# Performance work log

Hardware: AMD Instinct MI355X
Metric: run time of the kernel (lower is better)

## Reference

```python
import jax, jax.numpy as jnp
import numpy as np

N = 50000   # number of nodes
E = 25000   # number of hyperedges
IN = 256
OUT = 256
L = 32      # incidence list width (padded with 0)
NEG = -9e15  # matches torch's -9000000000000000.0 (fits in fp32)


def setup_inputs() -> dict:
    key = jax.random.key(0)
    k1, k2, k3, k4, k5 = jax.random.split(key, 5)
    x = jax.random.normal(k1, (N, IN), dtype=jnp.float32)
    seq = jax.random.randint(k2, (E, L), 0, N)      # node ids per hyperedge
    useq = jax.random.randint(k3, (N, L), 0, E)     # edge ids per node
    stdv = 1.0 / np.sqrt(IN)
    W1 = jax.random.uniform(k4, (IN, OUT), minval=-stdv, maxval=stdv, dtype=jnp.float32)
    W2 = jax.random.uniform(k5, (OUT, OUT), minval=-stdv, maxval=stdv, dtype=jnp.float32)
    return {"x": x, "seq": seq, "useq": useq, "W1": W1, "W2": W2}


def _mask_softmax_weights(idx):
    # softmax over where(idx>0, 1, -9e15): uniform weights over non-padding slots
    logits = jnp.where(idx > 0, 1.0, NEG).astype(jnp.float32)
    return jax.nn.softmax(logits, axis=1)


def reference(x, seq, useq, W1, W2):
    x1 = x @ W1                                   # [N, OUT]
    w = _mask_softmax_weights(seq)                # [E, L]
    edge = jnp.einsum('elc,el->ec', x1[seq], w)   # gather + weighted reduce -> [E, OUT]
    # F.dropout is identity in eval mode
    edge = jax.nn.relu(edge)
    e1 = edge @ W2                                # [E, OUT]
    uw = _mask_softmax_weights(useq)              # [N, L]
    node = jnp.einsum('nlc,nl->nc', e1[useq], uw) # [N, OUT]
    return node
```

## Files before the change

### kernel.cpp

```cpp
#include <hip/hip_runtime.h>

constexpr int N_NODES = 50000;
constexpr int N_EDGES = 25000;
constexpr int C = 256;
constexpr int L = 32;

__device__ ushort W1T_g[C * C];
__device__ ushort W2T_g[C * C];

__device__ __forceinline__ float bf2f(unsigned int h) {
    union { unsigned int u; float f; } c; c.u = h << 16; return c.f;
}
__device__ __forceinline__ ushort f2bf(float f) {
    union { float f; unsigned int u; } c; c.f = f;
    unsigned int r = c.u + 0x7FFFu + ((c.u >> 16) & 1u);
    return (ushort)(r >> 16);
}

__global__ __launch_bounds__(256) void convert_x_kernel(
    const float* __restrict__ x, ushort* __restrict__ xb)
{
    const size_t i = ((size_t)blockIdx.x * 256 + threadIdx.x) * 4;
    const float4 v = *reinterpret_cast<const float4*>(x + i);
    ushort4 o;
    o.x = f2bf(v.x); o.y = f2bf(v.y); o.z = f2bf(v.z); o.w = f2bf(v.w);
    *reinterpret_cast<ushort4*>(xb + i) = o;
}

__global__ __launch_bounds__(256) void wconv_kernel(
    const float* __restrict__ W1, const float* __restrict__ W2)
{
    const float* W  = blockIdx.z ? W2 : W1;
    ushort* WT      = blockIdx.z ? W2T_g : W1T_g;
    __shared__ float t[64][65];
    const int rr = threadIdx.x >> 6;
    const int cc = threadIdx.x & 63;
    const int br = blockIdx.x * 64;
    const int bc = blockIdx.y * 64;
#pragma unroll
    for (int i = 0; i < 16; ++i) {
        const int row = i * 4 + rr;
        t[row][cc] = W[(size_t)(br + row) * C + bc + cc];
    }
    __syncthreads();
#pragma unroll
    for (int i = 0; i < 16; ++i) {
        const int n = i * 4 + rr;
        WT[(size_t)(bc + n) * C + br + cc] = f2bf(t[cc][n]);
    }
}

template <typename OutT>
__global__ __launch_bounds__(256) void gather_avg_kernel(
    const ushort* __restrict__ src, const int* __restrict__ idx,
    OutT* __restrict__ dst, int nrows)
{
    const int row = blockIdx.x * 8 + (threadIdx.x >> 5);
    const int ln  = threadIdx.x & 31;
    if (row >= nrows) return;

    const int myid = idx[(size_t)row * L + ln];
    const unsigned long long b = __ballot(myid > 0);
    const unsigned int halfmask = (unsigned int)(b >> (threadIdx.x & 32));
    const int cnt = __popc(halfmask);
    const bool all = (cnt == 0);
    const float w = all ? (1.0f / (float)L) : (1.0f / (float)cnt);

    float acc[8] = {0.f, 0.f, 0.f, 0.f, 0.f, 0.f, 0.f, 0.f};
#pragma unroll 4
    for (int l = 0; l < L; ++l) {
        const int id = __shfl(myid, l, 32);
        if (all || id > 0) {
            const uint4 v = *reinterpret_cast<const uint4*>(
                src + (size_t)id * C + ln * 8);
            acc[0] += bf2f(v.x & 0xFFFFu); acc[1] += bf2f(v.x >> 16);
            acc[2] += bf2f(v.y & 0xFFFFu); acc[3] += bf2f(v.y >> 16);
            acc[4] += bf2f(v.z & 0xFFFFu); acc[5] += bf2f(v.z >> 16);
            acc[6] += bf2f(v.w & 0xFFFFu); acc[7] += bf2f(v.w >> 16);
        }
    }

    if constexpr (sizeof(OutT) == 2) {
        ushort* d = (ushort*)dst + (size_t)row * C + ln * 8;
        ushort4 o0, o1;
        o0.x = f2bf(acc[0] * w); o0.y = f2bf(acc[1] * w);
        o0.z = f2bf(acc[2] * w); o0.w = f2bf(acc[3] * w);
        o1.x = f2bf(acc[4] * w); o1.y = f2bf(acc[5] * w);
        o1.z = f2bf(acc[6] * w); o1.w = f2bf(acc[7] * w);
        *reinterpret_cast<ushort4*>(d)     = o0;
        *reinterpret_cast<ushort4*>(d + 4) = o1;
    } else {
        float* d = (float*)dst + (size_t)row * C + ln * 8;
        float4 o0 = {acc[0] * w, acc[1] * w, acc[2] * w, acc[3] * w};
        float4 o1 = {acc[4] * w, acc[5] * w, acc[6] * w, acc[7] * w};
        *reinterpret_cast<float4*>(d)     = o0;
        *reinterpret_cast<float4*>(d + 4) = o1;
    }
}

typedef __attribute__((ext_vector_type(8))) short bf16x8;
typedef __attribute__((ext_vector_type(4))) float f32x4;

template <bool RELU>
__global__ __launch_bounds__(256) void gemm_mfma_kernel(
    const ushort* __restrict__ A, int which_w,
    ushort* __restrict__ Cmat, int M)
{
    const ushort* __restrict__ BT = which_w ? W2T_g : W1T_g;
    const int wave = threadIdx.x >> 6;
    const int lane = threadIdx.x & 63;
    const int quad = lane >> 4;
    const int l16  = lane & 15;
    const int base = (blockIdx.x * 4 + wave) * 16;
    int mc = base + l16; if (mc > M - 1) mc = M - 1;

    f32x4 acc[16];
    const f32x4 zero = {0.f, 0.f, 0.f, 0.f};
#pragma unroll
    for (int t = 0; t < 16; ++t) acc[t] = zero;

    const ushort* arow = A  + (size_t)mc  * C + quad * 8;
    const ushort* brow = BT + (size_t)l16 * C + quad * 8;

#pragma unroll
    for (int k0 = 0; k0 < C; k0 += 32) {
        const bf16x8 a = *reinterpret_cast<const bf16x8*>(arow + k0);
#pragma unroll
        for (int t = 0; t < 16; ++t) {
            const bf16x8 b = *reinterpret_cast<const bf16x8*>(
                brow + (size_t)t * 16 * C + k0);
            acc[t] = __builtin_amdgcn_mfma_f32_16x16x32_bf16(a, b, acc[t], 0, 0, 0);
        }
    }

#pragma unroll
    for (int t = 0; t < 16; ++t) {
#pragma unroll
        for (int r = 0; r < 4; ++r) {
            const int gm = base + quad * 4 + r;
            if (gm < M) {
                float v = acc[t][r];
                if (RELU) v = fmaxf(v, 0.f);
                Cmat[(size_t)gm * C + t * 16 + l16] = f2bf(v);
            }
        }
    }
}

extern "C" void kernel_launch(void* const* d_in, const int* in_sizes, int n_in,
                              void* d_out, int out_size, void* d_ws, size_t ws_size,
                              hipStream_t stream) {
    const float* x    = (const float*)d_in[0];
    const int*   seq  = (const int*)d_in[1];
    const int*   useq = (const int*)d_in[2];
    const float* W1   = (const float*)d_in[3];
    const float* W2   = (const float*)d_in[4];
    float* out = (float*)d_out;

    ushort* xb   = (ushort*)d_ws;
    ushort* tmp1 = xb + (size_t)N_NODES * C;
    ushort* edge = tmp1 + (size_t)N_EDGES * C;

    convert_x_kernel<<<dim3((N_NODES * C) / (256 * 4)), dim3(256), 0, stream>>>(x, xb);
    wconv_kernel<<<dim3(4, 4, 2), dim3(256), 0, stream>>>(W1, W2);

    gather_avg_kernel<ushort><<<dim3(N_EDGES / 8), dim3(256), 0, stream>>>(
        xb, seq, tmp1, N_EDGES);

    const dim3 ggrid((N_EDGES + 63) / 64);
    gemm_mfma_kernel<true><<<ggrid, dim3(256), 0, stream>>>(tmp1, 0, edge, N_EDGES);
    gemm_mfma_kernel<false><<<ggrid, dim3(256), 0, stream>>>(edge, 1, tmp1, N_EDGES);

    gather_avg_kernel<float><<<dim3(N_NODES / 8), dim3(256), 0, stream>>>(
        tmp1, useq, out, N_NODES);
}
```

Measured before the change: 320.1 us.

## Split gather-average into column chunks with shared-memory index staging

```diff
diff --git a/kernel.cpp b/kernel.cpp
--- a/kernel.cpp
+++ b/kernel.cpp
@@ -50,47 +50,74 @@
     }
 }
 
-template <typename OutT>
-__global__ __launch_bounds__(256) void gather_avg_kernel(
+template <int CH, int NCHUNK, typename OutT>
+__global__ __launch_bounds__(256) void gather_chunk_kernel(
     const ushort* __restrict__ src, const int* __restrict__ idx,
     OutT* __restrict__ dst, int nrows)
 {
-    const int row = blockIdx.x * 8 + (threadIdx.x >> 5);
-    const int ln  = threadIdx.x & 31;
-    if (row >= nrows) return;
-
-    const int myid = idx[(size_t)row * L + ln];
-    const unsigned long long b = __ballot(myid > 0);
-    const unsigned int halfmask = (unsigned int)(b >> (threadIdx.x & 32));
-    const int cnt = __popc(halfmask);
-    const bool all = (cnt == 0);
-    const float w = all ? (1.0f / (float)L) : (1.0f / (float)cnt);
+    constexpr int LPR = CH / 8;
+    constexpr int RPB = 256 / LPR;
+    const int chunk = blockIdx.x & (NCHUNK - 1);
+    const int rb    = (int)(blockIdx.x / NCHUNK) * RPB;
+    const int t     = threadIdx.x;
+
+    __shared__ int sidx[RPB][33];
+    constexpr int TOT = RPB * L;
+#pragma unroll
+    for (int i = 0; i < TOT / 256; ++i) {
+        const int flat = i * 256 + t;
+        const int r = flat >> 5, l = flat & 31;
+        sidx[r][l] = (rb + r < nrows) ? idx[(size_t)(rb + r) * L + l] : 0;
+    }
+    __syncthreads();
+
+    const int r   = t / LPR;
+    const int ch  = chunk * CH + (t % LPR) * 8;
+    const int row = rb + r;
 
     float acc[8] = {0.f, 0.f, 0.f, 0.f, 0.f, 0.f, 0.f, 0.f};
+    int cnt = 0;
 #pragma unroll 4
     for (int l = 0; l < L; ++l) {
-        const int id = __shfl(myid, l, 32);
-        if (all || id > 0) {
+        const int id = sidx[r][l];
+        if (id > 0) {
+            ++cnt;
             const uint4 v = *reinterpret_cast<const uint4*>(
-                src + (size_t)id * C + ln * 8);
+                src + (size_t)id * C + ch);
             acc[0] += bf2f(v.x & 0xFFFFu); acc[1] += bf2f(v.x >> 16);
             acc[2] += bf2f(v.y & 0xFFFFu); acc[3] += bf2f(v.y >> 16);
             acc[4] += bf2f(v.z & 0xFFFFu); acc[5] += bf2f(v.z >> 16);
             acc[6] += bf2f(v.w & 0xFFFFu); acc[7] += bf2f(v.w >> 16);
         }
     }
-
+    if (row >= nrows) return;
+
+    if (cnt == 0) {
+        const uint4 v = *reinterpret_cast<const uint4*>(src + ch);
+        if constexpr (sizeof(OutT) == 2) {
+            *reinterpret_cast<uint4*>((ushort*)dst + (size_t)row * C + ch) = v;
+        } else {
+            float* d = (float*)dst + (size_t)row * C + ch;
+            float4 o0 = {bf2f(v.x & 0xFFFFu), bf2f(v.x >> 16),
+                         bf2f(v.y & 0xFFFFu), bf2f(v.y >> 16)};
+            float4 o1 = {bf2f(v.z & 0xFFFFu), bf2f(v.z >> 16),
+                         bf2f(v.w & 0xFFFFu), bf2f(v.w >> 16)};
+            *reinterpret_cast<float4*>(d)     = o0;
+            *reinterpret_cast<float4*>(d + 4) = o1;
+        }
+        return;
+    }
+
+    const float w = 1.0f / (float)cnt;
     if constexpr (sizeof(OutT) == 2) {
-        ushort* d = (ushort*)dst + (size_t)row * C + ln * 8;
-        ushort4 o0, o1;
-        o0.x = f2bf(acc[0] * w); o0.y = f2bf(acc[1] * w);
-        o0.z = f2bf(acc[2] * w); o0.w = f2bf(acc[3] * w);
-        o1.x = f2bf(acc[4] * w); o1.y = f2bf(acc[5] * w);
-        o1.z = f2bf(acc[6] * w); o1.w = f2bf(acc[7] * w);
-        *reinterpret_cast<ushort4*>(d)     = o0;
-        *reinterpret_cast<ushort4*>(d + 4) = o1;
+        uint4 o;
+        o.x = (unsigned)f2bf(acc[0] * w) | ((unsigned)f2bf(acc[1] * w) << 16);
+        o.y = (unsigned)f2bf(acc[2] * w) | ((unsigned)f2bf(acc[3] * w) << 16);
+        o.z = (unsigned)f2bf(acc[4] * w) | ((unsigned)f2bf(acc[5] * w) << 16);
+        o.w = (unsigned)f2bf(acc[6] * w) | ((unsigned)f2bf(acc[7] * w) << 16);
+        *reinterpret_cast<uint4*>((ushort*)dst + (size_t)row * C + ch) = o;
     } else {
-        float* d = (float*)dst + (size_t)row * C + ln * 8;
+        float* d = (float*)dst + (size_t)row * C + ch;
         float4 o0 = {acc[0] * w, acc[1] * w, acc[2] * w, acc[3] * w};
         float4 o1 = {acc[4] * w, acc[5] * w, acc[6] * w, acc[7] * w};
         *reinterpret_cast<float4*>(d)     = o0;
@@ -164,13 +191,15 @@
     convert_x_kernel<<<dim3((N_NODES * C) / (256 * 4)), dim3(256), 0, stream>>>(x, xb);
     wconv_kernel<<<dim3(4, 4, 2), dim3(256), 0, stream>>>(W1, W2);
 
-    gather_avg_kernel<ushort><<<dim3(N_EDGES / 8), dim3(256), 0, stream>>>(
+    const int rblk1 = (N_EDGES + 63) / 64;
+    gather_chunk_kernel<32, 8, ushort><<<dim3(8 * rblk1), dim3(256), 0, stream>>>(
         xb, seq, tmp1, N_EDGES);
 
     const dim3 ggrid((N_EDGES + 63) / 64);
     gemm_mfma_kernel<true><<<ggrid, dim3(256), 0, stream>>>(tmp1, 0, edge, N_EDGES);
     gemm_mfma_kernel<false><<<ggrid, dim3(256), 0, stream>>>(edge, 1, tmp1, N_EDGES);
 
-    gather_avg_kernel<float><<<dim3(N_NODES / 8), dim3(256), 0, stream>>>(
+    const int rblk2 = (N_NODES + 31) / 32;
+    gather_chunk_kernel<64, 4, float><<<dim3(4 * rblk2), dim3(256), 0, stream>>>(
         tmp1, useq, out, N_NODES);
 }
```

Result: faster. 308.3 us (-3.7%).

## Make gathers branchless with zero-row correction, chunk node gather, retile GEMM

Applied to the files above, without the earlier changes.

```diff
diff --git a/kernel.cpp b/kernel.cpp
--- a/kernel.cpp
+++ b/kernel.cpp
@@ -8,13 +8,22 @@
 __device__ ushort W1T_g[C * C];
 __device__ ushort W2T_g[C * C];
 
-__device__ __forceinline__ float bf2f(unsigned int h) {
-    union { unsigned int u; float f; } c; c.u = h << 16; return c.f;
-}
 __device__ __forceinline__ ushort f2bf(float f) {
     union { float f; unsigned int u; } c; c.f = f;
     unsigned int r = c.u + 0x7FFFu + ((c.u >> 16) & 1u);
     return (ushort)(r >> 16);
+}
+__device__ __forceinline__ float bflo(unsigned int u) {
+    union { unsigned int x; float f; } c; c.x = u << 16; return c.f;
+}
+__device__ __forceinline__ float bfhi(unsigned int u) {
+    union { unsigned int x; float f; } c; c.x = u & 0xFFFF0000u; return c.f;
+}
+__device__ __forceinline__ void acc_uint4(float* acc, const uint4 v) {
+    acc[0] += bflo(v.x); acc[1] += bfhi(v.x);
+    acc[2] += bflo(v.y); acc[3] += bfhi(v.y);
+    acc[4] += bflo(v.z); acc[5] += bfhi(v.z);
+    acc[6] += bflo(v.w); acc[7] += bfhi(v.w);
 }
 
 __global__ __launch_bounds__(256) void convert_x_kernel(
@@ -50,10 +59,9 @@
     }
 }
 
-template <typename OutT>
-__global__ __launch_bounds__(256) void gather_avg_kernel(
+__global__ __launch_bounds__(256) void gather_edge_kernel(
     const ushort* __restrict__ src, const int* __restrict__ idx,
-    OutT* __restrict__ dst, int nrows)
+    ushort* __restrict__ dst, int nrows)
 {
     const int row = blockIdx.x * 8 + (threadIdx.x >> 5);
     const int ln  = threadIdx.x & 31;
@@ -63,39 +71,86 @@
     const unsigned long long b = __ballot(myid > 0);
     const unsigned int halfmask = (unsigned int)(b >> (threadIdx.x & 32));
     const int cnt = __popc(halfmask);
-    const bool all = (cnt == 0);
-    const float w = all ? (1.0f / (float)L) : (1.0f / (float)cnt);
 
     float acc[8] = {0.f, 0.f, 0.f, 0.f, 0.f, 0.f, 0.f, 0.f};
-#pragma unroll 4
+#pragma unroll
     for (int l = 0; l < L; ++l) {
         const int id = __shfl(myid, l, 32);
-        if (all || id > 0) {
-            const uint4 v = *reinterpret_cast<const uint4*>(
-                src + (size_t)id * C + ln * 8);
-            acc[0] += bf2f(v.x & 0xFFFFu); acc[1] += bf2f(v.x >> 16);
-            acc[2] += bf2f(v.y & 0xFFFFu); acc[3] += bf2f(v.y >> 16);
-            acc[4] += bf2f(v.z & 0xFFFFu); acc[5] += bf2f(v.z >> 16);
-            acc[6] += bf2f(v.w & 0xFFFFu); acc[7] += bf2f(v.w >> 16);
-        }
-    }
-
-    if constexpr (sizeof(OutT) == 2) {
-        ushort* d = (ushort*)dst + (size_t)row * C + ln * 8;
-        ushort4 o0, o1;
-        o0.x = f2bf(acc[0] * w); o0.y = f2bf(acc[1] * w);
-        o0.z = f2bf(acc[2] * w); o0.w = f2bf(acc[3] * w);
-        o1.x = f2bf(acc[4] * w); o1.y = f2bf(acc[5] * w);
-        o1.z = f2bf(acc[6] * w); o1.w = f2bf(acc[7] * w);
-        *reinterpret_cast<ushort4*>(d)     = o0;
-        *reinterpret_cast<ushort4*>(d + 4) = o1;
-    } else {
-        float* d = (float*)dst + (size_t)row * C + ln * 8;
-        float4 o0 = {acc[0] * w, acc[1] * w, acc[2] * w, acc[3] * w};
-        float4 o1 = {acc[4] * w, acc[5] * w, acc[6] * w, acc[7] * w};
-        *reinterpret_cast<float4*>(d)     = o0;
-        *reinterpret_cast<float4*>(d + 4) = o1;
-    }
+        const uint4 v = *reinterpret_cast<const uint4*>(
+            src + (size_t)id * C + ln * 8);
+        acc_uint4(acc, v);
+    }
+    const uint4 v0 = *reinterpret_cast<const uint4*>(src + ln * 8);
+    float x0[8];
+    x0[0] = bflo(v0.x); x0[1] = bfhi(v0.x); x0[2] = bflo(v0.y); x0[3] = bfhi(v0.y);
+    x0[4] = bflo(v0.z); x0[5] = bfhi(v0.z); x0[6] = bflo(v0.w); x0[7] = bfhi(v0.w);
+
+    const float corr = (cnt == 0) ? 0.f : (float)(L - cnt);
+    const float inv  = (cnt == 0) ? (1.f / (float)L) : (1.f / (float)cnt);
+
+    ushort* d = dst + (size_t)row * C + ln * 8;
+    uint4 o;
+    o.x = (unsigned)f2bf((acc[0] - corr * x0[0]) * inv) |
+          ((unsigned)f2bf((acc[1] - corr * x0[1]) * inv) << 16);
+    o.y = (unsigned)f2bf((acc[2] - corr * x0[2]) * inv) |
+          ((unsigned)f2bf((acc[3] - corr * x0[3]) * inv) << 16);
+    o.z = (unsigned)f2bf((acc[4] - corr * x0[4]) * inv) |
+          ((unsigned)f2bf((acc[5] - corr * x0[5]) * inv) << 16);
+    o.w = (unsigned)f2bf((acc[6] - corr * x0[6]) * inv) |
+          ((unsigned)f2bf((acc[7] - corr * x0[7]) * inv) << 16);
+    *reinterpret_cast<uint4*>(d) = o;
+}
+
+__global__ __launch_bounds__(256) void gather_node_kernel(
+    const ushort* __restrict__ src, const int* __restrict__ idx,
+    float* __restrict__ dst, int nrows)
+{
+    constexpr int CH = 64, NCHUNK = 4;
+    constexpr int LPR = CH / 8;
+    constexpr int RPB = 256 / LPR;
+    const int chunk = blockIdx.x & (NCHUNK - 1);
+    const int rb    = (int)(blockIdx.x / NCHUNK) * RPB;
+    const int t     = threadIdx.x;
+
+    __shared__ int sidx[RPB][33];
+#pragma unroll
+    for (int i = 0; i < (RPB * L) / 256; ++i) {
+        const int flat = i * 256 + t;
+        const int r = flat >> 5, l = flat & 31;
+        sidx[r][l] = (rb + r < nrows) ? idx[(size_t)(rb + r) * L + l] : 0;
+    }
+    __syncthreads();
+
+    const int r   = t / LPR;
+    const int ch  = chunk * CH + (t % LPR) * 8;
+    const int row = rb + r;
+    if (row >= nrows) return;
+
+    float acc[8] = {0.f, 0.f, 0.f, 0.f, 0.f, 0.f, 0.f, 0.f};
+    int cnt = 0;
+#pragma unroll
+    for (int l = 0; l < L; ++l) {
+        const int id = sidx[r][l];
+        cnt += (id > 0) ? 1 : 0;
+        const uint4 v = *reinterpret_cast<const uint4*>(
+            src + (size_t)id * C + ch);
+        acc_uint4(acc, v);
+    }
+    const uint4 v0 = *reinterpret_cast<const uint4*>(src + ch);
+    float x0[8];
+    x0[0] = bflo(v0.x); x0[1] = bfhi(v0.x); x0[2] = bflo(v0.y); x0[3] = bfhi(v0.y);
+    x0[4] = bflo(v0.z); x0[5] = bfhi(v0.z); x0[6] = bflo(v0.w); x0[7] = bfhi(v0.w);
+
+    const float corr = (cnt == 0) ? 0.f : (float)(L - cnt);
+    const float inv  = (cnt == 0) ? (1.f / (float)L) : (1.f / (float)cnt);
+
+    float* d = dst + (size_t)row * C + ch;
+    float4 o0 = {(acc[0] - corr * x0[0]) * inv, (acc[1] - corr * x0[1]) * inv,
+                 (acc[2] - corr * x0[2]) * inv, (acc[3] - corr * x0[3]) * inv};
+    float4 o1 = {(acc[4] - corr * x0[4]) * inv, (acc[5] - corr * x0[5]) * inv,
+                 (acc[6] - corr * x0[6]) * inv, (acc[7] - corr * x0[7]) * inv};
+    *reinterpret_cast<float4*>(d)     = o0;
+    *reinterpret_cast<float4*>(d + 4) = o1;
 }
 
 typedef __attribute__((ext_vector_type(8))) short bf16x8;
@@ -107,42 +162,51 @@
     ushort* __restrict__ Cmat, int M)
 {
     const ushort* __restrict__ BT = which_w ? W2T_g : W1T_g;
-    const int wave = threadIdx.x >> 6;
-    const int lane = threadIdx.x & 63;
-    const int quad = lane >> 4;
-    const int l16  = lane & 15;
-    const int base = (blockIdx.x * 4 + wave) * 16;
-    int mc = base + l16; if (mc > M - 1) mc = M - 1;
-
-    f32x4 acc[16];
+    const int wave  = threadIdx.x >> 6;
+    const int lane  = threadIdx.x & 63;
+    const int quad  = lane >> 4;
+    const int l16   = lane & 15;
+    const int base  = (blockIdx.x * 4 + wave) * 32;
+    const int nbase = blockIdx.y * 128;
+
+    int m0 = base + l16;      if (m0 > M - 1) m0 = M - 1;
+    int m1 = base + 16 + l16; if (m1 > M - 1) m1 = M - 1;
+
+    f32x4 acc[2][8];
     const f32x4 zero = {0.f, 0.f, 0.f, 0.f};
 #pragma unroll
-    for (int t = 0; t < 16; ++t) acc[t] = zero;
-
-    const ushort* arow = A  + (size_t)mc  * C + quad * 8;
-    const ushort* brow = BT + (size_t)l16 * C + quad * 8;
+    for (int p = 0; p < 2; ++p)
+#pragma unroll
+        for (int t = 0; t < 8; ++t) acc[p][t] = zero;
+
+    const ushort* a0 = A + (size_t)m0 * C + quad * 8;
+    const ushort* a1 = A + (size_t)m1 * C + quad * 8;
+    const ushort* br = BT + (size_t)(nbase + l16) * C + quad * 8;
 
 #pragma unroll
     for (int k0 = 0; k0 < C; k0 += 32) {
-        const bf16x8 a = *reinterpret_cast<const bf16x8*>(arow + k0);
-#pragma unroll
-        for (int t = 0; t < 16; ++t) {
+        const bf16x8 av0 = *reinterpret_cast<const bf16x8*>(a0 + k0);
+        const bf16x8 av1 = *reinterpret_cast<const bf16x8*>(a1 + k0);
+#pragma unroll
+        for (int t = 0; t < 8; ++t) {
             const bf16x8 b = *reinterpret_cast<const bf16x8*>(
-                brow + (size_t)t * 16 * C + k0);
-            acc[t] = __builtin_amdgcn_mfma_f32_16x16x32_bf16(a, b, acc[t], 0, 0, 0);
+                br + (size_t)t * 16 * C + k0);
+            acc[0][t] = __builtin_amdgcn_mfma_f32_16x16x32_bf16(av0, b, acc[0][t], 0, 0, 0);
+            acc[1][t] = __builtin_amdgcn_mfma_f32_16x16x32_bf16(av1, b, acc[1][t], 0, 0, 0);
         }
     }
 
 #pragma unroll
-    for (int t = 0; t < 16; ++t) {
-#pragma unroll
-        for (int r = 0; r < 4; ++r) {
-            const int gm = base + quad * 4 + r;
-            if (gm < M) {
-                float v = acc[t][r];
-                if (RELU) v = fmaxf(v, 0.f);
-                Cmat[(size_t)gm * C + t * 16 + l16] = f2bf(v);
-            }
+    for (int p = 0; p < 2; ++p)
+#pragma unroll
+    for (int t = 0; t < 8; ++t)
+#pragma unroll
+    for (int r = 0; r < 4; ++r) {
+        const int gm = base + p * 16 + quad * 4 + r;
+        if (gm < M) {
+            float v = acc[p][t][r];
+            if (RELU) v = fmaxf(v, 0.f);
+            Cmat[(size_t)gm * C + nbase + t * 16 + l16] = f2bf(v);
         }
     }
 }
@@ -164,13 +228,14 @@
     convert_x_kernel<<<dim3((N_NODES * C) / (256 * 4)), dim3(256), 0, stream>>>(x, xb);
     wconv_kernel<<<dim3(4, 4, 2), dim3(256), 0, stream>>>(W1, W2);
 
-    gather_avg_kernel<ushort><<<dim3(N_EDGES / 8), dim3(256), 0, stream>>>(
+    gather_edge_kernel<<<dim3((N_EDGES + 7) / 8), dim3(256), 0, stream>>>(
         xb, seq, tmp1, N_EDGES);
 
-    const dim3 ggrid((N_EDGES + 63) / 64);
+    const dim3 ggrid((N_EDGES + 127) / 128, 2);
     gemm_mfma_kernel<true><<<ggrid, dim3(256), 0, stream>>>(tmp1, 0, edge, N_EDGES);
     gemm_mfma_kernel<false><<<ggrid, dim3(256), 0, stream>>>(edge, 1, tmp1, N_EDGES);
 
-    gather_avg_kernel<float><<<dim3(N_NODES / 8), dim3(256), 0, stream>>>(
+    const int rblk2 = (N_NODES + 31) / 32;
+    gather_node_kernel<<<dim3(4 * rblk2), dim3(256), 0, stream>>>(
         tmp1, useq, out, N_NODES);
 }
```

New measurement: 280.5 us. -12.4%, faster.
